# Kernel optimization log

Measured on AMD Instinct MI355X. Metric: run time of the kernel, lower is better.

The kernel has to match this reference:

```python
import jax, jax.numpy as jnp
import numpy as np

KERNEL_SIZE = 7      # odd, per assert in __init__
MAX_VAL = 1e4        # kornia morphology default max_val


def setup_inputs() -> dict:
    key = jax.random.key(0)
    kx, ka, kb, kc = jax.random.split(key, 4)
    x = jax.random.normal(kx, (8, 64, 256, 256), dtype=jnp.float32)
    k1 = jax.random.uniform(ka, (1,), dtype=jnp.float32)
    k2 = jax.random.uniform(kb, (1,), dtype=jnp.float32)
    k3 = jax.random.uniform(kc, (1,), dtype=jnp.float32)
    return {"x": x, "k1": k1, "k2": k2, "k3": k3}


def _structuring_element(k1, k2, k3):
    k = KERNEL_SIZE
    # torch.arange(-k//2 + 1, k//2 + 1) with floor-div == -(k//2)..k//2 for odd k
    c = jnp.arange(-(k // 2), k // 2 + 1, dtype=jnp.float32)
    xg, yg = jnp.meshgrid(c, c, indexing='xy')
    se = k1[0] * xg ** 2 + 2.0 * k2[0] * xg * yg + k3[0] * yg ** 2
    se = se / se.max()
    return -se  # (k, k)


def reference(x, k1, k2, k3):
    k = KERNEL_SIZE
    se = _structuring_element(k1, k2, k3)
    # flat kernel of ones with center zeroed -> center tap masked to -max_val
    mask = np.ones((k, k), dtype=bool)
    mask[k // 2, k // 2] = False
    neighborhood = jnp.where(jnp.asarray(mask), se, -MAX_VAL)
    nb = neighborhood[::-1, ::-1]  # kornia dilation flips the neighborhood

    pad = k // 2
    # geodesic border for dilation: pad with -max_val
    xp = jnp.pad(x, ((0, 0), (0, 0), (pad, pad), (pad, pad)),
                 constant_values=-MAX_VAL)
    H, W = x.shape[-2], x.shape[-1]
    # fused running max over the k*k taps; avoids materializing the unfold
    out = jnp.full_like(x, -jnp.inf)
    for i in range(k):
        for j in range(k):
            out = jnp.maximum(out, xp[..., i:i + H, j:j + W] + nb[i, j])
    return out
```

## Files before the change

kernel.cpp:

```cpp
#include <hip/hip_runtime.h>


#define MAXV 10000.0f

constexpr int H = 256;
constexpr int W = 256;
constexpr int SUB = 8;
constexpr int NSUB = 8;
constexpr int RING = 14;
constexpr int LSTR = 264;
constexpr int R = 2;

typedef float vf4 __attribute__((ext_vector_type(4)));
typedef float vf2 __attribute__((ext_vector_type(2)));

__global__ __launch_bounds__(256, 8) void morpho_kernel(
    const float* __restrict__ x,
    const float* __restrict__ k1p,
    const float* __restrict__ k2p,
    const float* __restrict__ k3p,
    float* __restrict__ out) {
  __shared__ __align__(16) float tile[RING * LSTR];

  const int tid = threadIdx.x;
  const int lane = tid & 63;
  const int wid = __builtin_amdgcn_readfirstlane(tid >> 6);
  const int p = blockIdx.x >> 2;
  const int ty0 = (blockIdx.x & 3) * 64;

  const float* __restrict__ xp = x + (size_t)p * (H * W);
  float* __restrict__ op = out + (size_t)p * (H * W);

  if (tid < RING * 8) {
    const int h = tid & 7;
    const int col = (h < 4) ? h : (256 + h);
    tile[(tid >> 3) * LSTR + col] = -MAXV;
  }

  for (int i = tid; i < RING * 64; i += 256) {
    const int r = i >> 6;
    const int c = i & 63;
    const int gy = ty0 - 3 + r;
    vf4 v;
    if (gy >= 0) {
      v = *reinterpret_cast<const vf4*>(&xp[gy * W + c * 4]);
    } else {
      v.x = v.y = v.z = v.w = -MAXV;
    }
    *reinterpret_cast<vf4*>(&tile[r * LSTR + 4 + c * 4]) = v;
  }

  const float k1v = k1p[0], k2v = k2p[0], k3v = k3p[0];
  const int ia = lane >> 3, ib = lane & 7;
  const float xg = (float)(((ib < 6) ? ib : 6) - 3);
  const float yg = (float)(((ia < 6) ? ia : 6) - 3);
  const float sev = k1v * (xg * xg) + 2.0f * k2v * (xg * yg) + k3v * (yg * yg);
  float mx = sev;
#pragma unroll
  for (int off = 32; off; off >>= 1) mx = fmaxf(mx, __shfl_xor(mx, off, 64));
  const float wv = 0.0f - sev * (1.0f / mx);

  vf2 wp[7][3];
  float w6[7];
#pragma unroll
  for (int d = 0; d < 7; ++d) {
#pragma unroll
    for (int m = 0; m < 3; ++m) {
      vf2 pr;
      pr.x = __int_as_float(__builtin_amdgcn_readlane(__float_as_int(wv), d * 8 + 2 * m));
      pr.y = __int_as_float(__builtin_amdgcn_readlane(__float_as_int(wv), d * 8 + 2 * m + 1));
      wp[d][m] = pr;
    }
    w6[d] = __int_as_float(__builtin_amdgcn_readlane(__float_as_int(wv), d * 8 + 6));
  }
  wp[3][1].y = -MAXV;

  __syncthreads();

  int rbase = 0;
  for (int s = 0; s < NSUB; ++s) {
    vf4 stg[R];
    if (s < NSUB - 1) {
#pragma unroll
      for (int j = 0; j < R; ++j) {
        const int gy = ty0 + 11 + SUB * s + wid * R + j;
        if (gy < H) {
          stg[j] = *reinterpret_cast<const vf4*>(&xp[gy * W + lane * 4]);
        } else {
          stg[j].x = stg[j].y = stg[j].z = stg[j].w = -MAXV;
        }
      }
    }

    int sb0 = rbase + wid * R;
    if (sb0 >= RING) sb0 -= RING;
    const float* baseA = &tile[sb0 * LSTR + lane * 4];
    const float* baseB = baseA - RING * LSTR;
    const int thresh = RING - sb0;

    float acc[R][4];
#pragma unroll
    for (int t = 0; t < R; ++t)
#pragma unroll
      for (int c = 0; c < 4; ++c) acc[t][c] = -INFINITY;

#pragma unroll
    for (int iy = 0; iy < R + 6; ++iy) {
      const float* rp = ((iy >= thresh) ? baseB : baseA) + iy * LSTR;
      const vf4 q0 = *reinterpret_cast<const vf4*>(rp);
      const vf4 q1 = *reinterpret_cast<const vf4*>(rp + 4);
      const vf4 q2 = *reinterpret_cast<const vf4*>(rp + 8);

      const vf2 O0 = __builtin_shufflevector(q0, q0, 1, 2);
      const vf2 O1 = __builtin_shufflevector(q0, q1, 3, 4);
      const vf2 O2 = __builtin_shufflevector(q1, q1, 1, 2);
      const vf2 O3 = __builtin_shufflevector(q1, q2, 3, 4);
      const vf2 E0 = __builtin_shufflevector(q0, q0, 2, 3);
      const vf2 E1 = __builtin_shufflevector(q1, q1, 0, 1);
      const vf2 E2 = __builtin_shufflevector(q1, q1, 2, 3);
      const vf2 E3 = __builtin_shufflevector(q2, q2, 0, 1);

      const vf2 P[4][3] = {{O0, O1, O2}, {E0, E1, E2}, {O1, O2, O3}, {E1, E2, E3}};
      const float T[4] = {q1.w, q2.x, q2.y, q2.z};

#pragma unroll
      for (int t = 0; t < R; ++t) {
        const int dyr = iy - t;
        if (dyr < 0 || dyr > 6) continue;
#pragma unroll
        for (int c = 0; c < 4; ++c) {
          const vf2 a = P[c][0] + wp[dyr][0];
          const vf2 b = P[c][1] + wp[dyr][1];
          const vf2 g = P[c][2] + wp[dyr][2];
          const float s6 = T[c] + w6[dyr];
          const float m0 = fmaxf(fmaxf(a.x, a.y), b.x);
          const float m1 = fmaxf(fmaxf(b.y, g.x), g.y);
          const float m2 = fmaxf(fmaxf(s6, m0), m1);
          acc[t][c] = fmaxf(acc[t][c], m2);
        }
      }
    }

#pragma unroll
    for (int t = 0; t < R; ++t) {
      const int gy = ty0 + SUB * s + wid * R + t;
      vf4 v;
      v.x = acc[t][0];
      v.y = acc[t][1];
      v.z = acc[t][2];
      v.w = acc[t][3];
      *reinterpret_cast<vf4*>(&op[gy * W + lane * 4]) = v;
    }

    __syncthreads();
    if (s < NSUB - 1) {
#pragma unroll
      for (int j = 0; j < R; ++j) {
        int sb = rbase + wid * R + j;
        if (sb >= RING) sb -= RING;
        *reinterpret_cast<vf4*>(&tile[sb * LSTR + 4 + lane * 4]) = stg[j];
      }
      __syncthreads();
    }

    rbase += SUB;
    if (rbase >= RING) rbase -= RING;
  }
}

extern "C" void kernel_launch(void* const* d_in, const int* in_sizes, int n_in,
                              void* d_out, int out_size, void* d_ws, size_t ws_size,
                              hipStream_t stream) {
  const float* x = (const float*)d_in[0];
  const float* k1 = (const float*)d_in[1];
  const float* k2 = (const float*)d_in[2];
  const float* k3 = (const float*)d_in[3];
  float* outp = (float*)d_out;

  const int planes = 8 * 64;
  const int blocks = planes * 4;
  morpho_kernel<<<dim3(blocks), dim3(256), 0, stream>>>(x, k1, k2, k3, outp);
}
```

Measured before the change: 245.7 us.

## Replace LDS ring buffer with direct global loads and register row blocking

Drops the shared-memory ring buffer, its barriers and the staged prefetch. Each wave now computes four output rows per pass, reading the ten needed input rows directly from global memory with overlapping vf4 loads and patching the left and right borders with -MAXV in registers. Output is written with nontemporal stores. This removes LDS traffic and synchronisation but relies on L1/L2 to absorb the roughly 3x redundant column loads and the 10-rows-per-4 vertical overlap.

Result: slower. 254.3 us (+3.5%).

```diff
diff --git a/kernel.cpp b/kernel.cpp
--- a/kernel.cpp
+++ b/kernel.cpp
@@ -5,11 +5,6 @@
 
 constexpr int H = 256;
 constexpr int W = 256;
-constexpr int SUB = 8;
-constexpr int NSUB = 8;
-constexpr int RING = 14;
-constexpr int LSTR = 264;
-constexpr int R = 2;
 
 typedef float vf4 __attribute__((ext_vector_type(4)));
 typedef float vf2 __attribute__((ext_vector_type(2)));
@@ -20,8 +15,6 @@
     const float* __restrict__ k2p,
     const float* __restrict__ k3p,
     float* __restrict__ out) {
-  __shared__ __align__(16) float tile[RING * LSTR];
-
   const int tid = threadIdx.x;
   const int lane = tid & 63;
   const int wid = __builtin_amdgcn_readfirstlane(tid >> 6);
@@ -30,25 +23,6 @@
 
   const float* __restrict__ xp = x + (size_t)p * (H * W);
   float* __restrict__ op = out + (size_t)p * (H * W);
-
-  if (tid < RING * 8) {
-    const int h = tid & 7;
-    const int col = (h < 4) ? h : (256 + h);
-    tile[(tid >> 3) * LSTR + col] = -MAXV;
-  }
-
-  for (int i = tid; i < RING * 64; i += 256) {
-    const int r = i >> 6;
-    const int c = i & 63;
-    const int gy = ty0 - 3 + r;
-    vf4 v;
-    if (gy >= 0) {
-      v = *reinterpret_cast<const vf4*>(&xp[gy * W + c * 4]);
-    } else {
-      v.x = v.y = v.z = v.w = -MAXV;
-    }
-    *reinterpret_cast<vf4*>(&tile[r * LSTR + 4 + c * 4]) = v;
-  }
 
   const float k1v = k1p[0], k2v = k2p[0], k3v = k3p[0];
   const int ia = lane >> 3, ib = lane & 7;
@@ -75,41 +49,37 @@
   }
   wp[3][1].y = -MAXV;
 
-  __syncthreads();
+  const bool l0 = (lane == 0);
+  const bool l63 = (lane == 63);
+  const int o1 = lane * 4;
+  const int o0 = l0 ? o1 : o1 - 4;
+  const int o2 = l63 ? o1 : o1 + 4;
 
-  int rbase = 0;
-  for (int s = 0; s < NSUB; ++s) {
-    vf4 stg[R];
-    if (s < NSUB - 1) {
+  for (int k = 0; k < 4; ++k) {
+    const int y0c = ty0 + 4 * wid + 16 * k;
+
+    float acc[4][4];
 #pragma unroll
-      for (int j = 0; j < R; ++j) {
-        const int gy = ty0 + 11 + SUB * s + wid * R + j;
-        if (gy < H) {
-          stg[j] = *reinterpret_cast<const vf4*>(&xp[gy * W + lane * 4]);
-        } else {
-          stg[j].x = stg[j].y = stg[j].z = stg[j].w = -MAXV;
-        }
-      }
-    }
-
-    int sb0 = rbase + wid * R;
-    if (sb0 >= RING) sb0 -= RING;
-    const float* baseA = &tile[sb0 * LSTR + lane * 4];
-    const float* baseB = baseA - RING * LSTR;
-    const int thresh = RING - sb0;
-
-    float acc[R][4];
-#pragma unroll
-    for (int t = 0; t < R; ++t)
+    for (int t = 0; t < 4; ++t)
 #pragma unroll
       for (int c = 0; c < 4; ++c) acc[t][c] = -INFINITY;
 
 #pragma unroll
-    for (int iy = 0; iy < R + 6; ++iy) {
-      const float* rp = ((iy >= thresh) ? baseB : baseA) + iy * LSTR;
-      const vf4 q0 = *reinterpret_cast<const vf4*>(rp);
-      const vf4 q1 = *reinterpret_cast<const vf4*>(rp + 4);
-      const vf4 q2 = *reinterpret_cast<const vf4*>(rp + 8);
+    for (int iy = 0; iy < 10; ++iy) {
+      const int r = y0c - 3 + iy;
+      if (r < 0 || r >= H) continue;
+      const float* __restrict__ rb = xp + r * W;
+
+      vf4 q0 = *reinterpret_cast<const vf4*>(rb + o0);
+      vf4 q1 = *reinterpret_cast<const vf4*>(rb + o1);
+      vf4 q2 = *reinterpret_cast<const vf4*>(rb + o2);
+
+      q0.y = l0 ? -MAXV : q0.y;
+      q0.z = l0 ? -MAXV : q0.z;
+      q0.w = l0 ? -MAXV : q0.w;
+      q2.x = l63 ? -MAXV : q2.x;
+      q2.y = l63 ? -MAXV : q2.y;
+      q2.z = l63 ? -MAXV : q2.z;
 
       const vf2 O0 = __builtin_shufflevector(q0, q0, 1, 2);
       const vf2 O1 = __builtin_shufflevector(q0, q1, 3, 4);
@@ -124,7 +94,7 @@
       const float T[4] = {q1.w, q2.x, q2.y, q2.z};
 
 #pragma unroll
-      for (int t = 0; t < R; ++t) {
+      for (int t = 0; t < 4; ++t) {
         const int dyr = iy - t;
         if (dyr < 0 || dyr > 6) continue;
 #pragma unroll
@@ -142,29 +112,15 @@
     }
 
 #pragma unroll
-    for (int t = 0; t < R; ++t) {
-      const int gy = ty0 + SUB * s + wid * R + t;
+    for (int t = 0; t < 4; ++t) {
       vf4 v;
       v.x = acc[t][0];
       v.y = acc[t][1];
       v.z = acc[t][2];
       v.w = acc[t][3];
-      *reinterpret_cast<vf4*>(&op[gy * W + lane * 4]) = v;
+      __builtin_nontemporal_store(
+          v, reinterpret_cast<vf4*>(&op[(y0c + t) * W + lane * 4]));
     }
-
-    __syncthreads();
-    if (s < NSUB - 1) {
-#pragma unroll
-      for (int j = 0; j < R; ++j) {
-        int sb = rbase + wid * R + j;
-        if (sb >= RING) sb -= RING;
-        *reinterpret_cast<vf4*>(&tile[sb * LSTR + 4 + lane * 4]) = stg[j];
-      }
-      __syncthreads();
-    }
-
-    rbase += SUB;
-    if (rbase >= RING) rbase -= RING;
   }
 }
 
```
